# Kernel optimization log

Hardware: AMD Instinct MI355X
Metric: run time of the kernel (lower is better)

Reference implementation:

```python
import jax, jax.numpy as jnp
import numpy as np

D_MODEL, H, KV, HD = 2048, 32, 8, 64  # head_dim = 64, RoPE half-dim = 32
B, L = 2, 2048
EPS = 1e-06


def apply_rope(t, cos, sin):
    # t: [b,l,h,hd]; cos/sin: [1,l,1,hd//2] (broadcast over batch and heads)
    dim = t.shape[-1] // 2
    cos = cos[..., :dim]
    sin = sin[..., :dim]
    x1, x2 = t[..., :dim], t[..., dim:]
    return jnp.concatenate([x1 * cos - x2 * sin, x2 * cos + x1 * sin], axis=-1)


def setup_inputs() -> dict:
    key = jax.random.key(0)
    ks = jax.random.split(key, 5)
    x = jax.random.normal(ks[0], (B, L, D_MODEL), dtype=jnp.float32)
    # true rotary tables, theta=10000
    half = HD // 2
    inv_freq = 1.0 / (10000.0 ** (jnp.arange(half, dtype=jnp.float32) / half))
    ang = jnp.arange(L, dtype=jnp.float32)[:, None] * inv_freq[None, :]  # [L, half]
    cos = jnp.cos(ang)[None, :, None, :]  # [1,L,1,half]
    sin = jnp.sin(ang)[None, :, None, :]
    s = 0.02
    Wq = jax.random.normal(ks[1], (D_MODEL, D_MODEL), dtype=jnp.float32) * s
    Wk = jax.random.normal(ks[2], (D_MODEL, KV * HD), dtype=jnp.float32) * s
    Wv = jax.random.normal(ks[3], (D_MODEL, KV * HD), dtype=jnp.float32) * s
    Wo = jax.random.normal(ks[4], (D_MODEL, D_MODEL), dtype=jnp.float32) * s
    return {"x": x, "cos": cos, "sin": sin, "Wq": Wq, "Wk": Wk, "Wv": Wv, "Wo": Wo}


def reference(x, cos, sin, Wq, Wk, Wv, Wo):
    b, l, _ = x.shape
    q = (x @ Wq).reshape(b, l, H, HD)
    k = (x @ Wk).reshape(b, l, KV, HD)
    v = (x @ Wv).reshape(b, l, KV, HD)
    q = apply_rope(q, cos, sin)
    k = apply_rope(k, cos[:, :, :KV, :], sin[:, :, :KV, :])
    # QK RMS-norm (qk_norm=True path), done in fp32
    q32 = q.astype(jnp.float32)
    k32 = k.astype(jnp.float32)
    q = (q32 * jax.lax.rsqrt(jnp.mean(jnp.square(q32), axis=-1, keepdims=True) + EPS)).astype(q.dtype)
    k = (k32 * jax.lax.rsqrt(jnp.mean(jnp.square(k32), axis=-1, keepdims=True) + EPS)).astype(k.dtype)
    # GQA: repeat KV heads to match Q heads
    g = H // KV
    k = jnp.repeat(k, g, axis=2)
    v = jnp.repeat(v, g, axis=2)
    scale = jax.lax.rsqrt(jnp.float32(HD))
    scores = jnp.einsum('blhd,bmhd->bhlm', q, k) * scale  # [b,H,L,L]
    causal = jnp.tril(jnp.ones((l, l), dtype=jnp.bool_))[None, None]
    scores = jnp.where(causal, scores, jnp.full_like(scores, -10000.0))
    attn = jax.nn.softmax(scores.astype(jnp.float32), axis=-1).astype(v.dtype)
    out = jnp.einsum('bhql,blhd->bqhd', attn, v).reshape(b, l, D_MODEL)
    return out @ Wo
```

## Files before the change

### kernel.cpp

```cpp
#include <hip/hip_runtime.h>
#include <hip/hip_bf16.h>
#include <cstdint>
#include <cstddef>

#define D_MODEL 2048
#define NH 32
#define NKV 8
#define HD 64
#define BB 2
#define LL 2048
#define EPS 1e-6f
#define MM (BB * LL)
#define QS 3072
#define KO 2048
#define VO 2560
#define QSCALE 0.18033688f
#define SM_BIAS 11.5415603f

typedef __hip_bfloat16 bf16;
typedef short bf16x8 __attribute__((ext_vector_type(8)));
typedef short s16x4 __attribute__((ext_vector_type(4)));
typedef float f32x4 __attribute__((ext_vector_type(4)));

__device__ inline float4 ld_bf4u(const unsigned short* p) {
  const ushort4 u = *(const ushort4*)p;
  float4 r;
  r.x = __uint_as_float(((unsigned)u.x) << 16);
  r.y = __uint_as_float(((unsigned)u.y) << 16);
  r.z = __uint_as_float(((unsigned)u.z) << 16);
  r.w = __uint_as_float(((unsigned)u.w) << 16);
  return r;
}
__device__ inline float4 ld4_rt(const void* p, size_t i, bool f32) {
  if (f32) return *(const float4*)((const float*)p + i);
  return ld_bf4u((const unsigned short*)p + i);
}
__device__ inline float ld1_rt(const void* p, size_t i, bool f32) {
  if (f32) return ((const float*)p)[i];
  unsigned short u = ((const unsigned short*)p)[i];
  return __uint_as_float(((unsigned)u) << 16);
}
__device__ inline unsigned short f2bf(float f) {
  bf16 h = __float2bfloat16(f);
  return *reinterpret_cast<unsigned short*>(&h);
}
__device__ inline float bfu2f(unsigned short u) {
  return __uint_as_float(((unsigned)u) << 16);
}
__device__ inline void store1(float* p, float v) { *p = v; }
__device__ inline void store1(unsigned short* p, float v) { *p = f2bf(v); }

__device__ inline void glds16(const unsigned short* g, unsigned short* l) {
  __builtin_amdgcn_global_load_lds(
      (const __attribute__((address_space(1))) unsigned int*)g,
      (__attribute__((address_space(3))) unsigned int*)l, 16, 0, 0);
}

__global__ __launch_bounds__(256) void detect_all(
    const unsigned short* p0, const unsigned short* p1, const unsigned short* p2,
    const unsigned short* p3, const unsigned short* p4, const unsigned short* p5,
    const unsigned short* p6, int* __restrict__ flags) {
  const unsigned short* ptrs[7] = {p0, p1, p2, p3, p4, p5, p6};
  const int b = blockIdx.x;
  const uint4* p = (const uint4*)ptrs[b];
  __shared__ int found;
  if (threadIdx.x == 0) found = 0;
  __syncthreads();
  int loc = 0;
#pragma unroll
  for (int it = 0; it < 16; ++it) {
    uint4 v = p[it * 256 + threadIdx.x];
    unsigned wds[4] = {v.x, v.y, v.z, v.w};
#pragma unroll
    for (int q = 0; q < 4; ++q) {
      unsigned lo = wds[q] & 0xFFFFu, hi = wds[q] >> 16;
      if (((lo >> 7) & 0xFFu) == 0xFFu || ((hi >> 7) & 0xFFu) == 0xFFu) loc = 1;
    }
  }
  if (loc) atomicOr(&found, 1);
  __syncthreads();
  if (threadIdx.x == 0) flags[b] = found;
}

__global__ __launch_bounds__(256) void cvt_bf16(const void* __restrict__ src,
                                                unsigned short* __restrict__ dst,
                                                int n4, const int* __restrict__ flags, int idx) {
  const bool f32 = flags[idx] != 0;
  int i = blockIdx.x * 256 + threadIdx.x;
  if (i < n4) {
    float4 v = ld4_rt(src, (size_t)i * 4, f32);
    ushort4 o;
    o.x = f2bf(v.x); o.y = f2bf(v.y); o.z = f2bf(v.z); o.w = f2bf(v.w);
    *(ushort4*)&dst[(size_t)i * 4] = o;
  }
}

__global__ __launch_bounds__(256) void transpose_all(
    const void* __restrict__ Wq, const void* __restrict__ Wk,
    const void* __restrict__ Wv, const void* __restrict__ Wo,
    unsigned short* __restrict__ WqkvT, unsigned short* __restrict__ WoT,
    const int* __restrict__ flags) {
  const int z = blockIdx.z;
  const void* srcs[4] = {Wq, Wk, Wv, Wo};
  unsigned short* dsts[4] = {WqkvT, WqkvT + (size_t)KO * 2048, WqkvT + (size_t)VO * 2048, WoT};
  const int Ns[4] = {2048, 512, 512, 2048};
  const int N = Ns[z];
  if (blockIdx.x * 64 >= N) return;
  const void* src = srcs[z];
  unsigned short* dst = dsts[z];
  const bool f32 = flags[3 + z] != 0;
  const int K = 2048;
  __shared__ unsigned short tile[64][65];
  const int t = threadIdx.x;
  const int n0 = blockIdx.x * 64, k0 = blockIdx.y * 64;
  const int cr = t >> 4, cc = (t & 15) * 4;
#pragma unroll
  for (int rr = 0; rr < 4; ++rr) {
    int row = rr * 16 + cr;
    float4 v = ld4_rt(src, (size_t)(k0 + row) * N + n0 + cc, f32);
    tile[row][cc + 0] = f2bf(v.x);
    tile[row][cc + 1] = f2bf(v.y);
    tile[row][cc + 2] = f2bf(v.z);
    tile[row][cc + 3] = f2bf(v.w);
  }
  __syncthreads();
#pragma unroll
  for (int rr = 0; rr < 4; ++rr) {
    int nrow = rr * 16 + cr;
    ushort4 o;
    o.x = tile[cc + 0][nrow];
    o.y = tile[cc + 1][nrow];
    o.z = tile[cc + 2][nrow];
    o.w = tile[cc + 3][nrow];
    *(ushort4*)&dst[(size_t)(n0 + nrow) * K + k0 + cc] = o;
  }
}

template <typename CT, int FUSE>
__global__ __launch_bounds__(256) void gemm_mfma(const unsigned short* __restrict__ A,
                                                 const unsigned short* __restrict__ Bt,
                                                 CT* __restrict__ C,
                                                 int M, int N, int K, int lda,
                                                 const void* __restrict__ cosp,
                                                 const void* __restrict__ sinp,
                                                 const int* __restrict__ flags,
                                                 unsigned short* __restrict__ vt) {
  __shared__ __align__(16) unsigned short As[3][128 * 32];
  __shared__ __align__(16) unsigned short Bs[3][128 * 32];
  const int t = threadIdx.x;
  const int lane = t & 63, w = t >> 6;
  const int wm = (w >> 1) * 64, wn = (w & 1) * 64;
  const int g = lane >> 4, m16 = lane & 15;
  const int nwg = gridDim.x * gridDim.y;
  const int orig = blockIdx.y * gridDim.x + blockIdx.x;
  const int swz = (orig & 7) * (nwg >> 3) + (orig >> 3);
  const int m0 = (swz / gridDim.x) * 128, n0 = (swz % gridDim.x) * 128;
  const int csw = (t & 3) ^ ((t >> 3) & 3);
  const unsigned short* gA = &A[(size_t)(m0 + (t >> 2)) * lda + csw * 8];
  const unsigned short* gB = &Bt[(size_t)(n0 + (t >> 2)) * K + csw * 8];
  const int l8 = t * 8;
  const int cs8 = (g ^ ((m16 >> 1) & 3)) * 8;
  f32x4 acc[4][4] = {};
  const int T = K >> 5;

#define STAGE(k0_, buf_)                                        \
  do {                                                          \
    glds16(gA + (k0_), &As[buf_][l8]);                          \
    glds16(gA + (size_t)64 * lda + (k0_), &As[buf_][l8 + 2048]);\
    glds16(gB + (k0_), &Bs[buf_][l8]);                          \
    glds16(gB + (size_t)64 * K + (k0_), &Bs[buf_][l8 + 2048]);  \
  } while (0)

  STAGE(0, 0);
  STAGE(32, 1);
  asm volatile("s_waitcnt vmcnt(4)" ::: "memory");
  __builtin_amdgcn_s_barrier();

  int buf = 0;
  for (int tt = 0; tt < T; ++tt) {
    const int k0 = tt << 5;
    if (tt + 2 < T) {
      int nb = buf + 2; if (nb >= 3) nb -= 3;
      STAGE(k0 + 64, nb);
    }
    bf16x8 af[4], bfr[4];
#pragma unroll
    for (int i = 0; i < 4; ++i) af[i] = *(const bf16x8*)&As[buf][(wm + i * 16 + m16) * 32 + cs8];
#pragma unroll
    for (int j = 0; j < 4; ++j) bfr[j] = *(const bf16x8*)&Bs[buf][(wn + j * 16 + m16) * 32 + cs8];
#pragma unroll
    for (int i = 0; i < 4; ++i)
#pragma unroll
      for (int j = 0; j < 4; ++j)
        acc[i][j] = __builtin_amdgcn_mfma_f32_16x16x32_bf16(af[i], bfr[j], acc[i][j], 0, 0, 0);
    if (tt + 1 < T) {
      if (tt + 2 < T) asm volatile("s_waitcnt vmcnt(4)" ::: "memory");
      else            asm volatile("s_waitcnt vmcnt(0)" ::: "memory");
      __builtin_amdgcn_s_barrier();
    }
    ++buf; if (buf >= 3) buf = 0;
  }
#undef STAGE

  if constexpr (FUSE) {
    const int colbase = n0 + wn;
    if (colbase < VO) {
      const bool cf = flags[1] != 0, sf = flags[2] != 0;
      const float post = (colbase < KO) ? QSCALE : 1.0f;
#pragma unroll
      for (int i = 0; i < 4; ++i)
#pragma unroll
        for (int r = 0; r < 4; ++r) {
          const int row = m0 + wm + i * 16 + g * 4 + r;
          const int l = row & (LL - 1);
          const float c0 = ld1_rt(cosp, l * 32 + m16, cf);
          const float c1 = ld1_rt(cosp, l * 32 + 16 + m16, cf);
          const float s0 = ld1_rt(sinp, l * 32 + m16, sf);
          const float s1 = ld1_rt(sinp, l * 32 + 16 + m16, sf);
          const float x0 = acc[i][0][r], x1 = acc[i][1][r];
          const float x2 = acc[i][2][r], x3 = acc[i][3][r];
          const float r0 = x0 * c0 - x2 * s0;
          const float r1 = x1 * c1 - x3 * s1;
          const float r2 = x2 * c0 + x0 * s0;
          const float r3 = x3 * c1 + x1 * s1;
          float ss = r0 * r0 + r1 * r1 + r2 * r2 + r3 * r3;
#pragma unroll
          for (int off = 1; off < 16; off <<= 1) ss += __shfl_xor(ss, off);
          const float sc = rsqrtf(ss * (1.0f / HD) + EPS) * post;
          CT* cr = &C[(size_t)row * N + colbase + m16];
          store1(cr + 0, r0 * sc);
          store1(cr + 16, r1 * sc);
          store1(cr + 32, r2 * sc);
          store1(cr + 48, r3 * sc);
        }
    } else {
      const int bb = (m0 + wm) >> 11;
      const int lb = (m0 + wm) & (LL - 1);
      const int kvh = (colbase - VO) >> 6;
      unsigned short* vb = vt + (size_t)(bb * NKV + kvh) * 64 * LL;
#pragma unroll
      for (int j = 0; j < 4; ++j)
#pragma unroll
        for (int i = 0; i < 4; ++i) {
          ushort4 pw;
          pw.x = f2bf(acc[i][j][0]); pw.y = f2bf(acc[i][j][1]);
          pw.z = f2bf(acc[i][j][2]); pw.w = f2bf(acc[i][j][3]);
          *(ushort4*)&vb[(size_t)(j * 16 + m16) * LL + lb + i * 16 + g * 4] = pw;
        }
    }
    return;
  }
#pragma unroll
  for (int i = 0; i < 4; ++i)
#pragma unroll
    for (int j = 0; j < 4; ++j)
#pragma unroll
      for (int r = 0; r < 4; ++r) {
        int row = m0 + wm + i * 16 + g * 4 + r;
        int col = n0 + wn + j * 16 + m16;
        store1(&C[(size_t)row * N + col], acc[i][j][r]);
      }
}

__global__ __launch_bounds__(256) void attn_mfma(unsigned short* __restrict__ qkv,
                                                 const unsigned short* __restrict__ vt) {
  __shared__ __align__(16) unsigned short Ks[2][64 * 64];
  __shared__ __align__(16) unsigned short Vs[2][64 * 64];
  __shared__ __align__(16) unsigned short Pt[4][64 * 16];
  const int t = threadIdx.x, lane = t & 63, w = t >> 6;
  const int g = lane >> 4, m16 = lane & 15;
  const int h = blockIdx.x, b = blockIdx.y;
  const int qt = (LL / 64 - 1) - blockIdx.z;
  const int kvh = h >> 2;
  const int q0 = qt * 64, qr0 = q0 + w * 16;

  bf16x8 qf0, qf1;
  {
    const unsigned short* qrow = &qkv[(size_t)(b * LL + qr0 + m16) * QS + h * 64 + g * 8];
    qf0 = *(const bf16x8*)&qrow[0];
    qf1 = *(const bf16x8*)&qrow[32];
  }
  f32x4 Oacc[4] = {};
  float lrow[4] = {0.f, 0.f, 0.f, 0.f};

  const int lr = lane >> 3;
  const int lc = (lane & 7) ^ lr;
  const unsigned short* gK = &qkv[(size_t)(b * LL) * QS + KO + kvh * 64 + lc * 8];
  const unsigned short* gV = &vt[((size_t)(b * NKV + kvh) * 64 + w * 16 + lr) * LL + lc * 8];
  const int dbase = w * 1024 + lane * 8;
  const int nIter = q0 / 64 + 1;

#pragma unroll
  for (int c = 0; c < 2; ++c) {
    glds16(gK + (size_t)(w * 16 + c * 8 + lr) * QS, &Ks[0][dbase + c * 512]);
    glds16(gV + (size_t)c * 8 * LL, &Vs[0][dbase + c * 512]);
  }
  __syncthreads();

  const int sw8 = (m16 & 7) * 8;
  for (int it = 0; it < nIter; ++it) {
    const int j0 = it * 64;
    const int cur = it & 1;
    if (it + 1 < nIter) {
      const int nj = j0 + 64;
#pragma unroll
      for (int c = 0; c < 2; ++c) {
        glds16(gK + (size_t)(nj + w * 16 + c * 8 + lr) * QS, &Ks[cur ^ 1][dbase + c * 512]);
        glds16(gV + (size_t)c * 8 * LL + nj, &Vs[cur ^ 1][dbase + c * 512]);
      }
    }
    const unsigned short* KsB = Ks[cur];
    const unsigned short* VsB = Vs[cur];

    f32x4 S[4];
#pragma unroll
    for (int jt = 0; jt < 4; ++jt) {
      const int rb = (jt * 16 + m16) * 64;
      bf16x8 kf0 = *(const bf16x8*)&KsB[rb + ((g * 8) ^ sw8)];
      bf16x8 kf1 = *(const bf16x8*)&KsB[rb + (((g + 4) * 8) ^ sw8)];
      f32x4 z = {0.f, 0.f, 0.f, 0.f};
      z = __builtin_amdgcn_mfma_f32_16x16x32_bf16(qf0, kf0, z, 0, 0, 0);
      S[jt] = __builtin_amdgcn_mfma_f32_16x16x32_bf16(qf1, kf1, z, 0, 0, 0);
    }
    if (j0 == q0) {
#pragma unroll
      for (int jt = 0; jt < 4; ++jt)
#pragma unroll
        for (int r = 0; r < 4; ++r) {
          int col = q0 + jt * 16 + m16;
          int row = qr0 + g * 4 + r;
          float p = __builtin_amdgcn_exp2f(S[jt][r] - SM_BIAS);
          p = (col <= row) ? p : 0.f;
          S[jt][r] = p;
          lrow[r] += p;
        }
    } else {
#pragma unroll
      for (int jt = 0; jt < 4; ++jt)
#pragma unroll
        for (int r = 0; r < 4; ++r) {
          float p = __builtin_amdgcn_exp2f(S[jt][r] - SM_BIAS);
          S[jt][r] = p;
          lrow[r] += p;
        }
    }
#pragma unroll
    for (int jt = 0; jt < 4; ++jt) {
      ushort4 pw;
      pw.x = f2bf(S[jt][0]); pw.y = f2bf(S[jt][1]);
      pw.z = f2bf(S[jt][2]); pw.w = f2bf(S[jt][3]);
      *(ushort4*)&Pt[w][(jt * 16 + m16) * 16 + g * 4] = pw;
    }
    s16x4 a0, a1, b0, b1;
    {
      __attribute__((address_space(3))) unsigned short* p3 =
          (__attribute__((address_space(3))) unsigned short*)&Pt[w][g * 128 + m16 * 4];
      unsigned paddr = (unsigned)(size_t)p3;
      asm volatile(
          "s_waitcnt lgkmcnt(0)\n\t"
          "ds_read_b64_tr_b16 %0, %4\n\t"
          "ds_read_b64_tr_b16 %1, %4 offset:128\n\t"
          "ds_read_b64_tr_b16 %2, %4 offset:1024\n\t"
          "ds_read_b64_tr_b16 %3, %4 offset:1152\n\t"
          "s_waitcnt lgkmcnt(0)"
          : "=&v"(a0), "=&v"(a1), "=&v"(b0), "=&v"(b1)
          : "v"(paddr)
          : "memory");
      __builtin_amdgcn_sched_barrier(0);
    }
    bf16x8 pf0 = __builtin_shufflevector(a0, a1, 0, 1, 2, 3, 4, 5, 6, 7);
    bf16x8 pf1 = __builtin_shufflevector(b0, b1, 0, 1, 2, 3, 4, 5, 6, 7);
#pragma unroll
    for (int dt = 0; dt < 4; ++dt) {
      const int rb = (dt * 16 + m16) * 64;
      bf16x8 vf0 = *(const bf16x8*)&VsB[rb + ((g * 8) ^ sw8)];
      bf16x8 vf1 = *(const bf16x8*)&VsB[rb + (((g + 4) * 8) ^ sw8)];
      Oacc[dt] = __builtin_amdgcn_mfma_f32_16x16x32_bf16(pf0, vf0, Oacc[dt], 0, 0, 0);
      Oacc[dt] = __builtin_amdgcn_mfma_f32_16x16x32_bf16(pf1, vf1, Oacc[dt], 0, 0, 0);
    }
    __syncthreads();
  }
  float inv[4];
#pragma unroll
  for (int r = 0; r < 4; ++r) {
#pragma unroll
    for (int off = 1; off < 16; off <<= 1) lrow[r] += __shfl_xor(lrow[r], off);
    inv[r] = 1.0f / lrow[r];
  }
#pragma unroll
  for (int dt = 0; dt < 4; ++dt)
#pragma unroll
    for (int r = 0; r < 4; ++r) {
      int row = qr0 + g * 4 + r;
      qkv[(size_t)(b * LL + row) * QS + h * 64 + dt * 16 + m16] = f2bf(Oacc[dt][r] * inv[r]);
    }
}

extern "C" void kernel_launch(void* const* d_in, const int* in_sizes, int n_in,
                              void* d_out, int out_size, void* d_ws, size_t ws_size,
                              hipStream_t stream) {
  const void* x = d_in[0];
  const void* cosp = d_in[1];
  const void* sinp = d_in[2];
  const void* Wq = d_in[3];
  const void* Wk = d_in[4];
  const void* Wv = d_in[5];
  const void* Wo = d_in[6];
  float* out = (float*)d_out;

  char* w0 = (char*)d_ws;
  int* flags = (int*)w0;
  unsigned short* xb = (unsigned short*)(w0 + 256);
  unsigned short* qkvb = xb + (size_t)MM * 2048;
  unsigned short* WqkvT = qkvb + (size_t)MM * QS;
  unsigned short* WoT = WqkvT + (size_t)QS * 2048;
  unsigned short* vt = WoT + (size_t)2048 * 2048;

  detect_all<<<7, 256, 0, stream>>>(
      (const unsigned short*)x, (const unsigned short*)cosp, (const unsigned short*)sinp,
      (const unsigned short*)Wq, (const unsigned short*)Wk, (const unsigned short*)Wv,
      (const unsigned short*)Wo, flags);
  cvt_bf16<<<MM * 2048 / 4 / 256, 256, 0, stream>>>(x, xb, MM * 2048 / 4, flags, 0);
  transpose_all<<<dim3(32, 32, 4), 256, 0, stream>>>(Wq, Wk, Wv, Wo, WqkvT, WoT, flags);
  gemm_mfma<unsigned short, 1><<<dim3(QS / 128, MM / 128), 256, 0, stream>>>(
      xb, WqkvT, qkvb, MM, QS, 2048, 2048, cosp, sinp, flags, vt);
  attn_mfma<<<dim3(NH, BB, LL / 64), 256, 0, stream>>>(qkvb, vt);
  gemm_mfma<float, 0><<<dim3(2048 / 128, MM / 128), 256, 0, stream>>>(
      qkvb, WoT, out, MM, 2048, 2048, QS, nullptr, nullptr, nullptr, nullptr);
}
```

Measured before the change: 317.1 us.

## Replace 128x128 GEMM with 256x256 tile, 8-wave ping-pong pipelined kernel

Both projection GEMMs now use 256x256 output tiles with 512 threads and BK=64 double-buffered LDS split into halves. Loads of the next K slice are interleaved with MFMA quarter-blocks, separated by scheduling barriers and s_setprio. This raises arithmetic intensity per byte loaded and overlaps global-to-LDS traffic with matrix math. The cost is fewer workgroups: 12x16=192 for QKV and 8x16=128 for the output projection, which can underfill 256 CUs. It also uses heavy register and LDS usage (128KB LDS).

```diff
diff --git a/kernel.cpp b/kernel.cpp
--- a/kernel.cpp
+++ b/kernel.cpp
@@ -137,81 +137,142 @@
 }
 
 template <typename CT, int FUSE>
-__global__ __launch_bounds__(256) void gemm_mfma(const unsigned short* __restrict__ A,
-                                                 const unsigned short* __restrict__ Bt,
-                                                 CT* __restrict__ C,
-                                                 int M, int N, int K, int lda,
-                                                 const void* __restrict__ cosp,
-                                                 const void* __restrict__ sinp,
-                                                 const int* __restrict__ flags,
-                                                 unsigned short* __restrict__ vt) {
-  __shared__ __align__(16) unsigned short As[3][128 * 32];
-  __shared__ __align__(16) unsigned short Bs[3][128 * 32];
+__global__ __launch_bounds__(512, 2) void gemm256(const unsigned short* __restrict__ A,
+                                                  const unsigned short* __restrict__ Bt,
+                                                  CT* __restrict__ C,
+                                                  int M, int N, int K, int lda,
+                                                  const void* __restrict__ cosp,
+                                                  const void* __restrict__ sinp,
+                                                  const int* __restrict__ flags,
+                                                  unsigned short* __restrict__ vt) {
+  __shared__ __align__(16) unsigned short LA[2][2][128 * 64];
+  __shared__ __align__(16) unsigned short LB[2][2][128 * 64];
   const int t = threadIdx.x;
   const int lane = t & 63, w = t >> 6;
-  const int wm = (w >> 1) * 64, wn = (w & 1) * 64;
+  const int wm = w >> 2;
+  const int wn = w & 3;
   const int g = lane >> 4, m16 = lane & 15;
+  const int sw = m16 & 7;
   const int nwg = gridDim.x * gridDim.y;
   const int orig = blockIdx.y * gridDim.x + blockIdx.x;
   const int swz = (orig & 7) * (nwg >> 3) + (orig >> 3);
-  const int m0 = (swz / gridDim.x) * 128, n0 = (swz % gridDim.x) * 128;
-  const int csw = (t & 3) ^ ((t >> 3) & 3);
-  const unsigned short* gA = &A[(size_t)(m0 + (t >> 2)) * lda + csw * 8];
-  const unsigned short* gB = &Bt[(size_t)(n0 + (t >> 2)) * K + csw * 8];
-  const int l8 = t * 8;
-  const int cs8 = (g ^ ((m16 >> 1) & 3)) * 8;
-  f32x4 acc[4][4] = {};
-  const int T = K >> 5;
-
-#define STAGE(k0_, buf_)                                        \
-  do {                                                          \
-    glds16(gA + (k0_), &As[buf_][l8]);                          \
-    glds16(gA + (size_t)64 * lda + (k0_), &As[buf_][l8 + 2048]);\
-    glds16(gB + (k0_), &Bs[buf_][l8]);                          \
-    glds16(gB + (size_t)64 * K + (k0_), &Bs[buf_][l8 + 2048]);  \
+  const int m0 = (swz / gridDim.x) * 256, n0 = (swz % gridDim.x) * 256;
+  const int grow = t >> 3;
+  const int gch = (t & 7) ^ (grow & 7);
+  const unsigned short* gA0 = A + (size_t)(m0 + grow) * lda + gch * 8;
+  const unsigned short* gA1 = A + (size_t)(m0 + 128 + grow) * lda + gch * 8;
+  const unsigned short* gB0 = Bt + (size_t)(n0 + grow) * K + gch * 8;
+  const unsigned short* gB1 = Bt + (size_t)(n0 + 128 + grow) * K + gch * 8;
+
+  f32x4 acc[8][4] = {};
+  bf16x8 a[4][2], b[4][2];
+
+#define STG(gp, stride, lp)                              \
+  do {                                                   \
+    glds16((gp), (lp) + t * 8);                          \
+    glds16((gp) + (size_t)64 * (stride), (lp) + 4096 + t * 8); \
   } while (0)
-
-  STAGE(0, 0);
-  STAGE(32, 1);
+#define LDA_(buf_, mh_)                                                          \
+  do {                                                                           \
+    const unsigned short* ab_ = &LA[buf_][wm][0];                                \
+    _Pragma("unroll") for (int i_ = 0; i_ < 4; ++i_) {                           \
+      const int row_ = ((mh_)*4 + i_) * 16 + m16;                                \
+      a[i_][0] = *(const bf16x8*)&ab_[row_ * 64 + ((g ^ sw) * 8)];               \
+      a[i_][1] = *(const bf16x8*)&ab_[row_ * 64 + (((4 + g) ^ sw) * 8)];         \
+    }                                                                            \
+  } while (0)
+#define LDB_(buf_, j_)                                                           \
+  do {                                                                           \
+    const unsigned short* bb_ = &LB[buf_][wn >> 1][0];                           \
+    const int row_ = (wn & 1) * 64 + (j_)*16 + m16;                              \
+    b[j_][0] = *(const bf16x8*)&bb_[row_ * 64 + ((g ^ sw) * 8)];                 \
+    b[j_][1] = *(const bf16x8*)&bb_[row_ * 64 + (((4 + g) ^ sw) * 8)];           \
+  } while (0)
+#define MFQ(mh_, nh_)                                                            \
+  do {                                                                           \
+    __builtin_amdgcn_s_setprio(1);                                               \
+    _Pragma("unroll") for (int i_ = 0; i_ < 4; ++i_)                             \
+      _Pragma("unroll") for (int jj_ = 0; jj_ < 2; ++jj_)                        \
+        _Pragma("unroll") for (int kk_ = 0; kk_ < 2; ++kk_)                      \
+          acc[(mh_)*4 + i_][(nh_)*2 + jj_] =                                     \
+              __builtin_amdgcn_mfma_f32_16x16x32_bf16(                           \
+                  a[i_][kk_], b[(nh_)*2 + jj_][kk_],                             \
+                  acc[(mh_)*4 + i_][(nh_)*2 + jj_], 0, 0, 0);                    \
+    __builtin_amdgcn_s_setprio(0);                                               \
+  } while (0)
+#define SBAR()                              \
+  do {                                      \
+    __builtin_amdgcn_sched_barrier(0);      \
+    __builtin_amdgcn_s_barrier();           \
+    __builtin_amdgcn_sched_barrier(0);      \
+  } while (0)
+
+  STG(gA0, lda, &LA[0][0][0]);
+  STG(gA1, lda, &LA[0][1][0]);
+  STG(gB0, K, &LB[0][0][0]);
+  STG(gB1, K, &LB[0][1][0]);
+  STG(gB0 + 64, K, &LB[1][0][0]);
+  STG(gB1 + 64, K, &LB[1][1][0]);
   asm volatile("s_waitcnt vmcnt(4)" ::: "memory");
-  __builtin_amdgcn_s_barrier();
-
-  int buf = 0;
-  for (int tt = 0; tt < T; ++tt) {
-    const int k0 = tt << 5;
-    if (tt + 2 < T) {
-      int nb = buf + 2; if (nb >= 3) nb -= 3;
-      STAGE(k0 + 64, nb);
-    }
-    bf16x8 af[4], bfr[4];
-#pragma unroll
-    for (int i = 0; i < 4; ++i) af[i] = *(const bf16x8*)&As[buf][(wm + i * 16 + m16) * 32 + cs8];
-#pragma unroll
-    for (int j = 0; j < 4; ++j) bfr[j] = *(const bf16x8*)&Bs[buf][(wn + j * 16 + m16) * 32 + cs8];
-#pragma unroll
-    for (int i = 0; i < 4; ++i)
-#pragma unroll
-      for (int j = 0; j < 4; ++j)
-        acc[i][j] = __builtin_amdgcn_mfma_f32_16x16x32_bf16(af[i], bfr[j], acc[i][j], 0, 0, 0);
-    if (tt + 1 < T) {
-      if (tt + 2 < T) asm volatile("s_waitcnt vmcnt(4)" ::: "memory");
-      else            asm volatile("s_waitcnt vmcnt(0)" ::: "memory");
-      __builtin_amdgcn_s_barrier();
-    }
-    ++buf; if (buf >= 3) buf = 0;
-  }
-#undef STAGE
-
+  SBAR();
+
+  const int NIT = K >> 7;
+  int kb = 64;
+  for (int it = 0; it < NIT; ++it) {
+    const bool more = (it + 1 < NIT);
+    const int kn = kb + 64;
+    const int knb = kb + 128;
+    LDA_(0, 0); LDB_(0, 0); LDB_(0, 1);
+    STG(gA0 + kb, lda, &LA[1][0][0]);
+    SBAR(); MFQ(0, 0); SBAR();
+    LDB_(0, 2); LDB_(0, 3);
+    STG(gA1 + kb, lda, &LA[1][1][0]);
+    SBAR(); MFQ(0, 1); SBAR();
+    LDA_(0, 1);
+    if (more) STG(gB0 + kn, K, &LB[0][0][0]);
+    SBAR(); MFQ(1, 1); SBAR();
+    if (more) {
+      STG(gB1 + kn, K, &LB[0][1][0]);
+      asm volatile("s_waitcnt vmcnt(4)" ::: "memory");
+    } else {
+      asm volatile("s_waitcnt vmcnt(0)" ::: "memory");
+    }
+    SBAR(); MFQ(1, 0); SBAR();
+    LDA_(1, 0); LDB_(1, 0); LDB_(1, 1);
+    if (more) STG(gA0 + kn, lda, &LA[0][0][0]);
+    SBAR(); MFQ(0, 0); SBAR();
+    LDB_(1, 2); LDB_(1, 3);
+    if (more) STG(gA1 + kn, lda, &LA[0][1][0]);
+    SBAR(); MFQ(0, 1); SBAR();
+    LDA_(1, 1);
+    if (more) STG(gB0 + knb, K, &LB[1][0][0]);
+    SBAR(); MFQ(1, 1); SBAR();
+    if (more) {
+      STG(gB1 + knb, K, &LB[1][1][0]);
+      asm volatile("s_waitcnt vmcnt(4)" ::: "memory");
+    } else {
+      asm volatile("s_waitcnt vmcnt(0)" ::: "memory");
+    }
+    SBAR(); MFQ(1, 0); SBAR();
+    kb += 128;
+  }
+#undef STG
+#undef LDA_
+#undef LDB_
+#undef MFQ
+#undef SBAR
+
+  const int rbase = m0 + wm * 128;
   if constexpr (FUSE) {
-    const int colbase = n0 + wn;
+    const int colbase = n0 + wn * 64;
     if (colbase < VO) {
       const bool cf = flags[1] != 0, sf = flags[2] != 0;
       const float post = (colbase < KO) ? QSCALE : 1.0f;
 #pragma unroll
-      for (int i = 0; i < 4; ++i)
+      for (int i = 0; i < 8; ++i)
 #pragma unroll
         for (int r = 0; r < 4; ++r) {
-          const int row = m0 + wm + i * 16 + g * 4 + r;
+          const int row = rbase + i * 16 + g * 4 + r;
           const int l = row & (LL - 1);
           const float c0 = ld1_rt(cosp, l * 32 + m16, cf);
           const float c1 = ld1_rt(cosp, l * 32 + 16 + m16, cf);
@@ -234,14 +295,14 @@
           store1(cr + 48, r3 * sc);
         }
     } else {
-      const int bb = (m0 + wm) >> 11;
-      const int lb = (m0 + wm) & (LL - 1);
+      const int bb = rbase >> 11;
+      const int lb = rbase & (LL - 1);
       const int kvh = (colbase - VO) >> 6;
       unsigned short* vb = vt + (size_t)(bb * NKV + kvh) * 64 * LL;
 #pragma unroll
       for (int j = 0; j < 4; ++j)
 #pragma unroll
-        for (int i = 0; i < 4; ++i) {
+        for (int i = 0; i < 8; ++i) {
           ushort4 pw;
           pw.x = f2bf(acc[i][j][0]); pw.y = f2bf(acc[i][j][1]);
           pw.z = f2bf(acc[i][j][2]); pw.w = f2bf(acc[i][j][3]);
@@ -251,13 +312,13 @@
     return;
   }
 #pragma unroll
-  for (int i = 0; i < 4; ++i)
+  for (int i = 0; i < 8; ++i)
 #pragma unroll
     for (int j = 0; j < 4; ++j)
 #pragma unroll
       for (int r = 0; r < 4; ++r) {
-        int row = m0 + wm + i * 16 + g * 4 + r;
-        int col = n0 + wn + j * 16 + m16;
+        int row = rbase + i * 16 + g * 4 + r;
+        int col = n0 + wn * 64 + j * 16 + m16;
         store1(&C[(size_t)row * N + col], acc[i][j][r]);
       }
 }
@@ -422,9 +483,9 @@
       (const unsigned short*)Wo, flags);
   cvt_bf16<<<MM * 2048 / 4 / 256, 256, 0, stream>>>(x, xb, MM * 2048 / 4, flags, 0);
   transpose_all<<<dim3(32, 32, 4), 256, 0, stream>>>(Wq, Wk, Wv, Wo, WqkvT, WoT, flags);
-  gemm_mfma<unsigned short, 1><<<dim3(QS / 128, MM / 128), 256, 0, stream>>>(
+  gemm256<unsigned short, 1><<<dim3(QS / 256, MM / 256), 512, 0, stream>>>(
       xb, WqkvT, qkvb, MM, QS, 2048, 2048, cosp, sinp, flags, vt);
   attn_mfma<<<dim3(NH, BB, LL / 64), 256, 0, stream>>>(qkvb, vt);
-  gemm_mfma<float, 0><<<dim3(2048 / 128, MM / 128), 256, 0, stream>>>(
+  gemm256<float, 0><<<dim3(2048 / 256, MM / 256), 512, 0, stream>>>(
       qkvb, WoT, out, MM, 2048, 2048, QS, nullptr, nullptr, nullptr, nullptr);
 }
```

Measured after the change: 335.2 us. 1.06x slower.

## Double-buffer GEMM register fragments and raise wave priority around attention MFMAs

Applied to the files above, without the earlier changes.

The GEMM main loop is unrolled by two. It ping-pongs two sets of register fragments so that LDS reads for the next k-tile overlap the MFMAs of the current tile, with the triple-buffered LDS rotated through offsets. This removes the stall between LDS fragment loads and MFMA issue within each iteration, at the cost of higher register pressure. In the attention kernel, s_setprio brackets the QK and PV MFMA blocks so that waves issuing matrix work get scheduling priority over waves doing softmax.

```diff
diff --git a/kernel.cpp b/kernel.cpp
--- a/kernel.cpp
+++ b/kernel.cpp
@@ -163,44 +163,54 @@
   f32x4 acc[4][4] = {};
   const int T = K >> 5;
 
-#define STAGE(k0_, buf_)                                        \
-  do {                                                          \
-    glds16(gA + (k0_), &As[buf_][l8]);                          \
-    glds16(gA + (size_t)64 * lda + (k0_), &As[buf_][l8 + 2048]);\
-    glds16(gB + (k0_), &Bs[buf_][l8]);                          \
-    glds16(gB + (size_t)64 * K + (k0_), &Bs[buf_][l8 + 2048]);  \
+#define STAGE(k0_, off_)                                                    \
+  do {                                                                      \
+    glds16(gA + (k0_), &As[0][0] + (off_) + l8);                            \
+    glds16(gA + (size_t)64 * lda + (k0_), &As[0][0] + (off_) + 2048 + l8);  \
+    glds16(gB + (k0_), &Bs[0][0] + (off_) + l8);                            \
+    glds16(gB + (size_t)64 * K + (k0_), &Bs[0][0] + (off_) + 2048 + l8);    \
   } while (0)
+#define LDF(fa_, fb_, off_)                                                               \
+  do {                                                                                    \
+    _Pragma("unroll") for (int i_ = 0; i_ < 4; ++i_)                                      \
+      fa_[i_] = *(const bf16x8*)(&As[0][0] + (off_) + (wm + i_ * 16 + m16) * 32 + cs8);   \
+    _Pragma("unroll") for (int j_ = 0; j_ < 4; ++j_)                                      \
+      fb_[j_] = *(const bf16x8*)(&Bs[0][0] + (off_) + (wn + j_ * 16 + m16) * 32 + cs8);   \
+  } while (0)
+#define MF(fa_, fb_)                                                   \
+  do {                                                                 \
+    _Pragma("unroll") for (int i_ = 0; i_ < 4; ++i_)                   \
+      _Pragma("unroll") for (int j_ = 0; j_ < 4; ++j_)                 \
+        acc[i_][j_] = __builtin_amdgcn_mfma_f32_16x16x32_bf16(         \
+            fa_[i_], fb_[j_], acc[i_][j_], 0, 0, 0);                   \
+  } while (0)
 
   STAGE(0, 0);
-  STAGE(32, 1);
+  STAGE(32, 4096);
   asm volatile("s_waitcnt vmcnt(4)" ::: "memory");
   __builtin_amdgcn_s_barrier();
-
-  int buf = 0;
-  for (int tt = 0; tt < T; ++tt) {
-    const int k0 = tt << 5;
-    if (tt + 2 < T) {
-      int nb = buf + 2; if (nb >= 3) nb -= 3;
-      STAGE(k0 + 64, nb);
-    }
-    bf16x8 af[4], bfr[4];
-#pragma unroll
-    for (int i = 0; i < 4; ++i) af[i] = *(const bf16x8*)&As[buf][(wm + i * 16 + m16) * 32 + cs8];
-#pragma unroll
-    for (int j = 0; j < 4; ++j) bfr[j] = *(const bf16x8*)&Bs[buf][(wn + j * 16 + m16) * 32 + cs8];
-#pragma unroll
-    for (int i = 0; i < 4; ++i)
-#pragma unroll
-      for (int j = 0; j < 4; ++j)
-        acc[i][j] = __builtin_amdgcn_mfma_f32_16x16x32_bf16(af[i], bfr[j], acc[i][j], 0, 0, 0);
-    if (tt + 1 < T) {
-      if (tt + 2 < T) asm volatile("s_waitcnt vmcnt(4)" ::: "memory");
-      else            asm volatile("s_waitcnt vmcnt(0)" ::: "memory");
-      __builtin_amdgcn_s_barrier();
-    }
-    ++buf; if (buf >= 3) buf = 0;
+  bf16x8 a0[4], b0[4], a1[4], b1[4];
+  LDF(a0, b0, 0);
+  int cur = 0, pf = 4096, st = 8192;
+  for (int tt = 0; tt < T; tt += 2) {
+    if (tt + 2 < T) STAGE((tt + 2) << 5, st);
+    if (tt + 3 < T) asm volatile("s_waitcnt vmcnt(4)" ::: "memory");
+    else            asm volatile("s_waitcnt vmcnt(0)" ::: "memory");
+    LDF(a1, b1, pf);
+    MF(a0, b0);
+    __builtin_amdgcn_s_barrier();
+    { int tmp = cur; cur = pf; pf = st; st = tmp; }
+    if (tt + 3 < T) STAGE((tt + 3) << 5, st);
+    if (tt + 4 < T) asm volatile("s_waitcnt vmcnt(4)" ::: "memory");
+    else            asm volatile("s_waitcnt vmcnt(0)" ::: "memory");
+    if (tt + 2 < T) LDF(a0, b0, pf);
+    MF(a1, b1);
+    if (tt + 2 < T) __builtin_amdgcn_s_barrier();
+    { int tmp = cur; cur = pf; pf = st; st = tmp; }
   }
 #undef STAGE
+#undef LDF
+#undef MF
 
   if constexpr (FUSE) {
     const int colbase = n0 + wn;
@@ -313,6 +323,7 @@
     const unsigned short* VsB = Vs[cur];
 
     f32x4 S[4];
+    __builtin_amdgcn_s_setprio(1);
 #pragma unroll
     for (int jt = 0; jt < 4; ++jt) {
       const int rb = (jt * 16 + m16) * 64;
@@ -322,6 +333,7 @@
       z = __builtin_amdgcn_mfma_f32_16x16x32_bf16(qf0, kf0, z, 0, 0, 0);
       S[jt] = __builtin_amdgcn_mfma_f32_16x16x32_bf16(qf1, kf1, z, 0, 0, 0);
     }
+    __builtin_amdgcn_s_setprio(0);
     if (j0 == q0) {
 #pragma unroll
       for (int jt = 0; jt < 4; ++jt)
@@ -370,6 +382,7 @@
     }
     bf16x8 pf0 = __builtin_shufflevector(a0, a1, 0, 1, 2, 3, 4, 5, 6, 7);
     bf16x8 pf1 = __builtin_shufflevector(b0, b1, 0, 1, 2, 3, 4, 5, 6, 7);
+    __builtin_amdgcn_s_setprio(1);
 #pragma unroll
     for (int dt = 0; dt < 4; ++dt) {
       const int rb = (dt * 16 + m16) * 64;
@@ -378,6 +391,7 @@
       Oacc[dt] = __builtin_amdgcn_mfma_f32_16x16x32_bf16(pf0, vf0, Oacc[dt], 0, 0, 0);
       Oacc[dt] = __builtin_amdgcn_mfma_f32_16x16x32_bf16(pf1, vf1, Oacc[dt], 0, 0, 0);
     }
+    __builtin_amdgcn_s_setprio(0);
     __syncthreads();
   }
   float inv[4];
```

Result: slower. 365.2 us (+15.2%).

## Share K/V tiles across GQA head group in one attention block

Applied to the files above, without the earlier changes.

The attention kernel now launches one block per KV head instead of per query head. Each of the four warps handles one query head of the GQA group across all 64 query rows, so each K/V tile staged in shared memory is reused by four heads. This cuts redundant global K/V loads fourfold and adds s_setprio around the MFMA sections. In exchange the grid shrinks fourfold, per-thread accumulator and register state grows about fourfold (which may reduce occupancy or spill), and the P staging buffer in shared memory grows.

```diff
diff --git a/kernel.cpp b/kernel.cpp
--- a/kernel.cpp
+++ b/kernel.cpp
@@ -266,22 +266,23 @@
                                                  const unsigned short* __restrict__ vt) {
   __shared__ __align__(16) unsigned short Ks[2][64 * 64];
   __shared__ __align__(16) unsigned short Vs[2][64 * 64];
-  __shared__ __align__(16) unsigned short Pt[4][64 * 16];
+  __shared__ __align__(16) unsigned short Pt[4][64 * 64];
   const int t = threadIdx.x, lane = t & 63, w = t >> 6;
   const int g = lane >> 4, m16 = lane & 15;
-  const int h = blockIdx.x, b = blockIdx.y;
+  const int kvh = blockIdx.x, b = blockIdx.y;
   const int qt = (LL / 64 - 1) - blockIdx.z;
-  const int kvh = h >> 2;
-  const int q0 = qt * 64, qr0 = q0 + w * 16;
-
-  bf16x8 qf0, qf1;
-  {
-    const unsigned short* qrow = &qkv[(size_t)(b * LL + qr0 + m16) * QS + h * 64 + g * 8];
-    qf0 = *(const bf16x8*)&qrow[0];
-    qf1 = *(const bf16x8*)&qrow[32];
-  }
-  f32x4 Oacc[4] = {};
-  float lrow[4] = {0.f, 0.f, 0.f, 0.f};
+  const int h = kvh * 4 + w;
+  const int q0 = qt * 64;
+
+  bf16x8 qf[4][2];
+#pragma unroll
+  for (int i = 0; i < 4; ++i) {
+    const unsigned short* qrow = &qkv[(size_t)(b * LL + q0 + i * 16 + m16) * QS + h * 64 + g * 8];
+    qf[i][0] = *(const bf16x8*)&qrow[0];
+    qf[i][1] = *(const bf16x8*)&qrow[32];
+  }
+  f32x4 Oacc[4][4] = {};
+  float lrow[4][4] = {};
 
   const int lr = lane >> 3;
   const int lc = (lane & 7) ^ lr;
@@ -312,88 +313,111 @@
     const unsigned short* KsB = Ks[cur];
     const unsigned short* VsB = Vs[cur];
 
-    f32x4 S[4];
+    f32x4 S[4][4];
+    __builtin_amdgcn_s_setprio(1);
 #pragma unroll
     for (int jt = 0; jt < 4; ++jt) {
       const int rb = (jt * 16 + m16) * 64;
       bf16x8 kf0 = *(const bf16x8*)&KsB[rb + ((g * 8) ^ sw8)];
       bf16x8 kf1 = *(const bf16x8*)&KsB[rb + (((g + 4) * 8) ^ sw8)];
-      f32x4 z = {0.f, 0.f, 0.f, 0.f};
-      z = __builtin_amdgcn_mfma_f32_16x16x32_bf16(qf0, kf0, z, 0, 0, 0);
-      S[jt] = __builtin_amdgcn_mfma_f32_16x16x32_bf16(qf1, kf1, z, 0, 0, 0);
-    }
+#pragma unroll
+      for (int i = 0; i < 4; ++i) {
+        f32x4 z = {0.f, 0.f, 0.f, 0.f};
+        z = __builtin_amdgcn_mfma_f32_16x16x32_bf16(qf[i][0], kf0, z, 0, 0, 0);
+        S[i][jt] = __builtin_amdgcn_mfma_f32_16x16x32_bf16(qf[i][1], kf1, z, 0, 0, 0);
+      }
+    }
+    __builtin_amdgcn_s_setprio(0);
     if (j0 == q0) {
 #pragma unroll
-      for (int jt = 0; jt < 4; ++jt)
-#pragma unroll
-        for (int r = 0; r < 4; ++r) {
-          int col = q0 + jt * 16 + m16;
-          int row = qr0 + g * 4 + r;
-          float p = __builtin_amdgcn_exp2f(S[jt][r] - SM_BIAS);
-          p = (col <= row) ? p : 0.f;
-          S[jt][r] = p;
-          lrow[r] += p;
-        }
+      for (int i = 0; i < 4; ++i)
+#pragma unroll
+        for (int jt = 0; jt < 4; ++jt)
+#pragma unroll
+          for (int r = 0; r < 4; ++r) {
+            int col = q0 + jt * 16 + m16;
+            int row = q0 + i * 16 + g * 4 + r;
+            float p = __builtin_amdgcn_exp2f(S[i][jt][r] - SM_BIAS);
+            p = (col <= row) ? p : 0.f;
+            S[i][jt][r] = p;
+            lrow[i][r] += p;
+          }
     } else {
 #pragma unroll
-      for (int jt = 0; jt < 4; ++jt)
-#pragma unroll
-        for (int r = 0; r < 4; ++r) {
-          float p = __builtin_amdgcn_exp2f(S[jt][r] - SM_BIAS);
-          S[jt][r] = p;
-          lrow[r] += p;
-        }
-    }
-#pragma unroll
-    for (int jt = 0; jt < 4; ++jt) {
-      ushort4 pw;
-      pw.x = f2bf(S[jt][0]); pw.y = f2bf(S[jt][1]);
-      pw.z = f2bf(S[jt][2]); pw.w = f2bf(S[jt][3]);
-      *(ushort4*)&Pt[w][(jt * 16 + m16) * 16 + g * 4] = pw;
-    }
-    s16x4 a0, a1, b0, b1;
-    {
+      for (int i = 0; i < 4; ++i)
+#pragma unroll
+        for (int jt = 0; jt < 4; ++jt)
+#pragma unroll
+          for (int r = 0; r < 4; ++r) {
+            float p = __builtin_amdgcn_exp2f(S[i][jt][r] - SM_BIAS);
+            S[i][jt][r] = p;
+            lrow[i][r] += p;
+          }
+    }
+#pragma unroll
+    for (int i = 0; i < 4; ++i)
+#pragma unroll
+      for (int jt = 0; jt < 4; ++jt) {
+        ushort4 pw;
+        pw.x = f2bf(S[i][jt][0]); pw.y = f2bf(S[i][jt][1]);
+        pw.z = f2bf(S[i][jt][2]); pw.w = f2bf(S[i][jt][3]);
+        *(ushort4*)&Pt[w][i * 1024 + (jt * 16 + m16) * 16 + g * 4] = pw;
+      }
+    s16x4 ta[4], tb[4], tc[4], td[4];
+    asm volatile("s_waitcnt lgkmcnt(0)" ::: "memory");
+#pragma unroll
+    for (int i = 0; i < 4; ++i) {
       __attribute__((address_space(3))) unsigned short* p3 =
-          (__attribute__((address_space(3))) unsigned short*)&Pt[w][g * 128 + m16 * 4];
+          (__attribute__((address_space(3))) unsigned short*)&Pt[w][i * 1024 + g * 128 + m16 * 4];
       unsigned paddr = (unsigned)(size_t)p3;
       asm volatile(
-          "s_waitcnt lgkmcnt(0)\n\t"
           "ds_read_b64_tr_b16 %0, %4\n\t"
           "ds_read_b64_tr_b16 %1, %4 offset:128\n\t"
           "ds_read_b64_tr_b16 %2, %4 offset:1024\n\t"
-          "ds_read_b64_tr_b16 %3, %4 offset:1152\n\t"
-          "s_waitcnt lgkmcnt(0)"
-          : "=&v"(a0), "=&v"(a1), "=&v"(b0), "=&v"(b1)
-          : "v"(paddr)
-          : "memory");
-      __builtin_amdgcn_sched_barrier(0);
-    }
-    bf16x8 pf0 = __builtin_shufflevector(a0, a1, 0, 1, 2, 3, 4, 5, 6, 7);
-    bf16x8 pf1 = __builtin_shufflevector(b0, b1, 0, 1, 2, 3, 4, 5, 6, 7);
+          "ds_read_b64_tr_b16 %3, %4 offset:1152"
+          : "=&v"(ta[i]), "=&v"(tb[i]), "=&v"(tc[i]), "=&v"(td[i])
+          : "v"(paddr));
+    }
+    asm volatile("s_waitcnt lgkmcnt(0)" ::: "memory");
+    __builtin_amdgcn_sched_barrier(0);
+    bf16x8 pf[4][2];
+#pragma unroll
+    for (int i = 0; i < 4; ++i) {
+      pf[i][0] = __builtin_shufflevector(ta[i], tb[i], 0, 1, 2, 3, 4, 5, 6, 7);
+      pf[i][1] = __builtin_shufflevector(tc[i], td[i], 0, 1, 2, 3, 4, 5, 6, 7);
+    }
+    __builtin_amdgcn_s_setprio(1);
 #pragma unroll
     for (int dt = 0; dt < 4; ++dt) {
       const int rb = (dt * 16 + m16) * 64;
       bf16x8 vf0 = *(const bf16x8*)&VsB[rb + ((g * 8) ^ sw8)];
       bf16x8 vf1 = *(const bf16x8*)&VsB[rb + (((g + 4) * 8) ^ sw8)];
-      Oacc[dt] = __builtin_amdgcn_mfma_f32_16x16x32_bf16(pf0, vf0, Oacc[dt], 0, 0, 0);
-      Oacc[dt] = __builtin_amdgcn_mfma_f32_16x16x32_bf16(pf1, vf1, Oacc[dt], 0, 0, 0);
-    }
+#pragma unroll
+      for (int i = 0; i < 4; ++i) {
+        Oacc[i][dt] = __builtin_amdgcn_mfma_f32_16x16x32_bf16(pf[i][0], vf0, Oacc[i][dt], 0, 0, 0);
+        Oacc[i][dt] = __builtin_amdgcn_mfma_f32_16x16x32_bf16(pf[i][1], vf1, Oacc[i][dt], 0, 0, 0);
+      }
+    }
+    __builtin_amdgcn_s_setprio(0);
     __syncthreads();
   }
-  float inv[4];
-#pragma unroll
-  for (int r = 0; r < 4; ++r) {
-#pragma unroll
-    for (int off = 1; off < 16; off <<= 1) lrow[r] += __shfl_xor(lrow[r], off);
-    inv[r] = 1.0f / lrow[r];
-  }
-#pragma unroll
-  for (int dt = 0; dt < 4; ++dt)
+#pragma unroll
+  for (int i = 0; i < 4; ++i) {
+    float inv[4];
 #pragma unroll
     for (int r = 0; r < 4; ++r) {
-      int row = qr0 + g * 4 + r;
-      qkv[(size_t)(b * LL + row) * QS + h * 64 + dt * 16 + m16] = f2bf(Oacc[dt][r] * inv[r]);
-    }
+#pragma unroll
+      for (int off = 1; off < 16; off <<= 1) lrow[i][r] += __shfl_xor(lrow[i][r], off);
+      inv[r] = 1.0f / lrow[i][r];
+    }
+#pragma unroll
+    for (int dt = 0; dt < 4; ++dt)
+#pragma unroll
+      for (int r = 0; r < 4; ++r) {
+        int row = q0 + i * 16 + g * 4 + r;
+        qkv[(size_t)(b * LL + row) * QS + h * 64 + dt * 16 + m16] = f2bf(Oacc[i][dt][r] * inv[r]);
+      }
+  }
 }
 
 extern "C" void kernel_launch(void* const* d_in, const int* in_sizes, int n_in,
@@ -424,7 +448,7 @@
   transpose_all<<<dim3(32, 32, 4), 256, 0, stream>>>(Wq, Wk, Wv, Wo, WqkvT, WoT, flags);
   gemm_mfma<unsigned short, 1><<<dim3(QS / 128, MM / 128), 256, 0, stream>>>(
       xb, WqkvT, qkvb, MM, QS, 2048, 2048, cosp, sinp, flags, vt);
-  attn_mfma<<<dim3(NH, BB, LL / 64), 256, 0, stream>>>(qkvb, vt);
+  attn_mfma<<<dim3(NKV, BB, LL / 64), 256, 0, stream>>>(qkvb, vt);
   gemm_mfma<float, 0><<<dim3(2048 / 128, MM / 128), 256, 0, stream>>>(
       qkvb, WoT, out, MM, 2048, 2048, QS, nullptr, nullptr, nullptr, nullptr);
 }
```

Result: slower. 330.4 us (+4.2%).
